# Performance work log

Hardware: AMD Instinct MI355X
Metric: run time of the kernel (lower is better)

Reference implementation:

```python
import jax, jax.numpy as jnp
import numpy as np

PAD = 1      # init_kwargs: padding
STRIDE = 1   # init_kwargs: stride


def setup_inputs() -> dict:
    key = jax.random.key(0)
    k1, k2 = jax.random.split(key)
    # x: [C=4, H=4096, W=4096] input feature map (no batch dim in original module)
    x = jax.random.normal(k1, (4, 4096, 4096), dtype=jnp.float32)
    # kernel: [cout=4, cin=4, h=3, w=3] learned conv weight (nn.Parameter)
    kernel = jax.random.normal(k2, (4, 4, 3, 3), dtype=jnp.float32)
    return {"x": x, "kernel": kernel}


def reference(x, kernel):
    # Faithful math: zero-pad by PAD on all four spatial sides, then a direct
    # cross-correlation (torch conv semantics) with stride STRIDE.
    # Original loops over output pixels; here it's a single fused conv primitive.
    out = jax.lax.conv_general_dilated(
        x[None],                      # [1, C, H, W]
        kernel,                       # [cout, cin, h, w]
        window_strides=(STRIDE, STRIDE),
        padding=[(PAD, PAD), (PAD, PAD)],
        dimension_numbers=("NCHW", "OIHW", "NCHW"),
    )
    return out[0]                     # [cout, hout, wout]
```

## Files before the change

kernel.cpp:

```cpp
#include <hip/hip_runtime.h>


#define IW 4096
#define IH 4096
constexpr long long HWsz = (long long)IH * IW;

typedef float v4f __attribute__((ext_vector_type(4)));

__device__ __forceinline__ void gload_lds16(const float* g, float* l) {
    __builtin_amdgcn_global_load_lds(
        (const __attribute__((address_space(1))) char*)g,
        (__attribute__((address_space(3))) char*)l, 16, 0, 0);
}

__device__ __forceinline__ void stage(const float* __restrict__ xin, int ci,
                                      float (*rbuf)[512], int y0, int X0,
                                      int w, int l) {
    const float* plane = xin + (long long)ci * HWsz;
    #pragma unroll
    for (int k = 0; k < 5; ++k) {
        const int c = 5 * w + k;
        const int r = c >> 1;
        const int h = c & 1;
        int yy = y0 - 1 + r;
        int yc = yy < 0 ? 0 : (yy >= IH ? IH - 1 : yy);
        gload_lds16(plane + (long long)yc * IW + (X0 + 256 * h + 4 * l),
                    &rbuf[r][256 * h]);
    }
}

__device__ __forceinline__ void compute_ci(float acc[4][4][4],
                                           const float (*rbuf)[512],
                                           const float* __restrict__ xin,
                                           const float* __restrict__ wt,
                                           int ci, int y0, int X0,
                                           int p_u, int tx) {
    const float* plane = xin + (long long)ci * HWsz;
    #pragma unroll
    for (int dy = 0; dy < 6; ++dy) {
        const int r  = 4 * p_u + dy;
        const int yy = y0 - 1 + r;
        if (yy >= 0 && yy < IH) {
            const float hL = (X0 > 0)
                ? plane[(long long)yy * IW + X0 - 1]   : 0.f;
            const float hR = (X0 + 512 < IW)
                ? plane[(long long)yy * IW + X0 + 512] : 0.f;
            const v4f a = *reinterpret_cast<const v4f*>(&rbuf[r][4 * tx]);
            const float L = (tx == 0)   ? hL : rbuf[r][4 * tx - 1];
            const float R = (tx == 127) ? hR : rbuf[r][4 * tx + 4];
            float vv[6] = {L, a.x, a.y, a.z, a.w, R};
            #pragma unroll
            for (int rk = 0; rk < 3; ++rk) {
                const int o = dy - rk;
                if (o >= 0 && o < 4) {
                    #pragma unroll
                    for (int co = 0; co < 4; ++co) {
                        #pragma unroll
                        for (int kx = 0; kx < 3; ++kx) {
                            const float w = wt[((co * 4 + ci) * 3 + rk) * 3 + kx];
                            #pragma unroll
                            for (int p = 0; p < 4; ++p)
                                acc[o][co][p] = fmaf(w, vv[p + kx], acc[o][co][p]);
                        }
                    }
                }
            }
        }
    }
}

__global__ __launch_bounds__(256) void conv3x3_kernel(
    const float* __restrict__ xin,
    const float* __restrict__ wt,
    float* __restrict__ out)
{
    __shared__ __align__(16) float rows[2][10][512];

    const int bid = blockIdx.x;
    const int swz = (bid & 7) * 512 + (bid >> 3);
    const int rowblk = swz >> 3;
    const int xs     = swz & 7;
    const int y0     = rowblk << 3;
    const int X0     = xs << 9;
    const int t      = (int)threadIdx.x;
    const int w      = t >> 6, l = t & 63;
    const int tx     = t & 127;
    const int p_u    = __builtin_amdgcn_readfirstlane(t >> 7);

    float acc[4][4][4];
    #pragma unroll
    for (int o = 0; o < 4; ++o)
        #pragma unroll
        for (int co = 0; co < 4; ++co)
            #pragma unroll
            for (int p = 0; p < 4; ++p) acc[o][co][p] = 0.f;

    stage(xin, 0, rows[0], y0, X0, w, l);

    #pragma unroll 1
    for (int ci = 0; ci < 4; ++ci) {
        const int cur = ci & 1;
        if (ci < 3) {
            stage(xin, ci + 1, rows[cur ^ 1], y0, X0, w, l);
            asm volatile("s_waitcnt vmcnt(5)\n\ts_barrier" ::: "memory");
        } else {
            asm volatile("s_waitcnt vmcnt(0)\n\ts_barrier" ::: "memory");
        }
        compute_ci(acc, rows[cur], xin, wt, ci, y0, X0, p_u, tx);
        if (ci < 3)
            asm volatile("s_barrier" ::: "memory");
    }

    const int x0g = X0 + 4 * tx;
    #pragma unroll
    for (int o = 0; o < 4; ++o) {
        const long long obase = (long long)(y0 + 4 * p_u + o) * IW + x0g;
        #pragma unroll
        for (int co = 0; co < 4; ++co) {
            v4f ov;
            ov.x = acc[o][co][0]; ov.y = acc[o][co][1];
            ov.z = acc[o][co][2]; ov.w = acc[o][co][3];
            __builtin_nontemporal_store(ov,
                reinterpret_cast<v4f*>(out + co * HWsz + obase));
        }
    }
}

extern "C" void kernel_launch(void* const* d_in, const int* in_sizes, int n_in,
                              void* d_out, int out_size, void* d_ws, size_t ws_size,
                              hipStream_t stream) {
    const float* xin = (const float*)d_in[0];
    const float* wt  = (const float*)d_in[1];
    float* out       = (float*)d_out;

    dim3 grid(4096), block(256);
    hipLaunchKernelGGL(conv3x3_kernel, grid, block, 0, stream, xin, wt, out);
}
```

Before: 95.79 us.

## Make blocks persistent over four row tiles with a continuous cross-tile prefetch pipeline

Each block now handles a 32-row band in four 8-row tiles instead of one, and runs a 16-phase loop that double-buffers channel loads across tile boundaries. Output stores are interleaved into the loop and the accumulators are reset after each tile. The grid shrinks from 4096 to 1024 blocks. The aim is to remove per-block prologue and epilogue latency and keep loads in flight across tiles. In exchange there are fewer blocks to hide latency, and the vmcnt(21) wait after store phases assumes a specific count of outstanding memory operations.

```diff
diff --git a/kernel.cpp b/kernel.cpp
--- a/kernel.cpp
+++ b/kernel.cpp
@@ -13,9 +13,11 @@
         (__attribute__((address_space(3))) char*)l, 16, 0, 0);
 }
 
-__device__ __forceinline__ void stage(const float* __restrict__ xin, int ci,
-                                      float (*rbuf)[512], int y0, int X0,
-                                      int w, int l) {
+__device__ __forceinline__ void stage_phase(const float* __restrict__ xin,
+                                            int f, float (*rbuf)[512],
+                                            int ybase, int X0, int w, int l) {
+    const int ci   = f & 3;
+    const int y0   = ybase + (f >> 2) * 8;
     const float* plane = xin + (long long)ci * HWsz;
     #pragma unroll
     for (int k = 0; k < 5; ++k) {
@@ -76,16 +78,16 @@
 {
     __shared__ __align__(16) float rows[2][10][512];
 
-    const int bid = blockIdx.x;
-    const int swz = (bid & 7) * 512 + (bid >> 3);
-    const int rowblk = swz >> 3;
-    const int xs     = swz & 7;
-    const int y0     = rowblk << 3;
-    const int X0     = xs << 9;
-    const int t      = (int)threadIdx.x;
-    const int w      = t >> 6, l = t & 63;
-    const int tx     = t & 127;
-    const int p_u    = __builtin_amdgcn_readfirstlane(t >> 7);
+    const int bid   = blockIdx.x;
+    const int g     = (bid & 7) * 128 + (bid >> 3);
+    const int band  = g >> 3;
+    const int strip = g & 7;
+    const int ybase = band << 5;
+    const int X0    = strip << 9;
+    const int t     = (int)threadIdx.x;
+    const int w     = t >> 6, l = t & 63;
+    const int tx    = t & 127;
+    const int p_u   = __builtin_amdgcn_readfirstlane(t >> 7);
 
     float acc[4][4][4];
     #pragma unroll
@@ -95,34 +97,47 @@
             #pragma unroll
             for (int p = 0; p < 4; ++p) acc[o][co][p] = 0.f;
 
-    stage(xin, 0, rows[0], y0, X0, w, l);
+    stage_phase(xin, 0, rows[0], ybase, X0, w, l);
 
     #pragma unroll 1
-    for (int ci = 0; ci < 4; ++ci) {
-        const int cur = ci & 1;
-        if (ci < 3) {
-            stage(xin, ci + 1, rows[cur ^ 1], y0, X0, w, l);
-            asm volatile("s_waitcnt vmcnt(5)\n\ts_barrier" ::: "memory");
+    for (int p = 0; p < 16; ++p) {
+        const int cur = p & 1;
+        if (p < 15) {
+            stage_phase(xin, p + 1, rows[cur ^ 1], ybase, X0, w, l);
+            if (p > 0 && (p & 3) == 0) {
+                asm volatile("s_waitcnt vmcnt(21)\n\ts_barrier" ::: "memory");
+            } else {
+                asm volatile("s_waitcnt vmcnt(5)\n\ts_barrier" ::: "memory");
+            }
         } else {
             asm volatile("s_waitcnt vmcnt(0)\n\ts_barrier" ::: "memory");
         }
+
+        const int ci = p & 3;
+        const int y0 = ybase + (p >> 2) * 8;
         compute_ci(acc, rows[cur], xin, wt, ci, y0, X0, p_u, tx);
-        if (ci < 3)
+
+        if (ci == 3) {
+            const int x0g = X0 + 4 * tx;
+            #pragma unroll
+            for (int o = 0; o < 4; ++o) {
+                const long long obase =
+                    (long long)(y0 + 4 * p_u + o) * IW + x0g;
+                #pragma unroll
+                for (int co = 0; co < 4; ++co) {
+                    v4f ov;
+                    ov.x = acc[o][co][0]; ov.y = acc[o][co][1];
+                    ov.z = acc[o][co][2]; ov.w = acc[o][co][3];
+                    __builtin_nontemporal_store(ov,
+                        reinterpret_cast<v4f*>(out + co * HWsz + obase));
+                    acc[o][co][0] = 0.f; acc[o][co][1] = 0.f;
+                    acc[o][co][2] = 0.f; acc[o][co][3] = 0.f;
+                }
+            }
+        }
+
+        if (p < 15)
             asm volatile("s_barrier" ::: "memory");
-    }
-
-    const int x0g = X0 + 4 * tx;
-    #pragma unroll
-    for (int o = 0; o < 4; ++o) {
-        const long long obase = (long long)(y0 + 4 * p_u + o) * IW + x0g;
-        #pragma unroll
-        for (int co = 0; co < 4; ++co) {
-            v4f ov;
-            ov.x = acc[o][co][0]; ov.y = acc[o][co][1];
-            ov.z = acc[o][co][2]; ov.w = acc[o][co][3];
-            __builtin_nontemporal_store(ov,
-                reinterpret_cast<v4f*>(out + co * HWsz + obase));
-        }
     }
 }
 
@@ -133,6 +148,6 @@
     const float* wt  = (const float*)d_in[1];
     float* out       = (float*)d_out;
 
-    dim3 grid(4096), block(256);
+    dim3 grid(1024), block(256);
     hipLaunchKernelGGL(conv3x3_kernel, grid, block, 0, stream, xin, wt, out);
 }
```

Measured after the change: 112.4 us. 1.17x slower.
